# Optimization experiments

Hardware: AMD Instinct MI355X
Metric: run time of the kernel (lower is better)

## Reference

```python
import jax, jax.numpy as jnp
import numpy as np

B, IN_DIM, HID, OUT_DIM = 32768, 784, 256, 1000
L, CURV = 3, 1e-3
LOG2_H = 8  # log2(HID)
EPS_BN = 1e-5

def _layer_param_sizes():
    return [(HID // (2 * (1 << (l % LOG2_H)))) * 2 for l in range(L)]

def setup_inputs():
    key = jax.random.key(0)
    ks = jax.random.split(key, 4)
    total = sum(_layer_param_sizes())  # 448
    return {
        "x": jax.random.normal(ks[0], (B, IN_DIM), jnp.float32),
        "fc1_w": jax.random.normal(ks[1], (HID, IN_DIM), jnp.float32) / np.sqrt(IN_DIM).astype(np.float32),
        "fc1_b": jnp.zeros((HID,), jnp.float32),
        "bn1_gamma": jnp.ones((HID,), jnp.float32),
        "bn1_beta": jnp.zeros((HID,), jnp.float32),
        "bf_params": jax.random.normal(ks[2], (total,), jnp.float32) * 0.01,
        "bn2_gamma": jnp.ones((HID,), jnp.float32),
        "bn2_beta": jnp.zeros((HID,), jnp.float32),
        "fc2_w": jax.random.normal(ks[3], (OUT_DIM, HID), jnp.float32) / np.sqrt(HID).astype(np.float32),
        "fc2_b": jnp.zeros((OUT_DIM,), jnp.float32),
    }

def _batchnorm(h, gamma, beta):
    # training-mode BatchNorm1d: batch mean / biased variance
    mu = jnp.mean(h, axis=0)
    var = jnp.mean(jnp.square(h - mu), axis=0)
    return gamma * (h - mu) * jax.lax.rsqrt(var + EPS_BN) + beta

def _log_map0(x, c):
    # Poincare ball log map at origin: artanh(sqrt(c)|x|) * x / (sqrt(c)|x|)
    sn = jnp.sqrt(c) * jnp.linalg.norm(x, axis=-1, keepdims=True)
    sn = jnp.clip(sn, 1e-7, 1.0 - 1e-6)
    return (jnp.arctanh(sn) / sn) * x

def _exp_map0(u, c):
    sn = jnp.maximum(jnp.sqrt(c) * jnp.linalg.norm(u, axis=-1, keepdims=True), 1e-7)
    return (jnp.tanh(sn) / sn) * u

def _hyper_butterfly(h, params, c):
    u = _log_map0(h, c)
    off = 0
    for l in range(L):
        bs = 1 << (l % LOG2_H)      # half-block size at stage l
        nb = HID // (2 * bs)        # number of 2x2-rotation blocks
        p = params[off:off + 2 * nb]
        a = p[:nb][None, :, None]   # [1, nb, 1]
        b = p[nb:][None, :, None]
        v = u.reshape(-1, nb, 2, bs)
        x1, x2 = v[:, :, 0], v[:, :, 1]
        y1 = a * x1 + b * x2
        y2 = -b * x1 + a * x2
        u = jnp.stack([y1, y2], axis=2).reshape(-1, HID)
        off += 2 * nb
    return _exp_map0(u, c)

def reference(x, fc1_w, fc1_b, bn1_gamma, bn1_beta, bf_params, bn2_gamma, bn2_beta, fc2_w, fc2_b):
    h = x @ fc1_w.T + fc1_b
    h = jax.nn.relu(_batchnorm(h, bn1_gamma, bn1_beta))
    ht = _hyper_butterfly(h, bf_params, CURV)
    ht = jax.nn.relu(_batchnorm(ht, bn2_gamma, bn2_beta))
    return ht @ fc2_w.T + fc2_b
```

## Files before the change

kernel.cpp:

```cpp
#include <hip/hip_runtime.h>
#include <math.h>

#define NBATCH 32768
#define IND    784
#define KPAD1  800
#define HIDD   256
#define OUTD   1000
#define OUTDP  1024

typedef _Float16 half8  __attribute__((ext_vector_type(8)));
typedef _Float16 half4v __attribute__((ext_vector_type(4)));
typedef float    floatx4 __attribute__((ext_vector_type(4)));

#define GAS __attribute__((address_space(1)))
#define LAS __attribute__((address_space(3)))

#define WAITVM(N) asm volatile("s_waitcnt vmcnt(" #N ")" ::: "memory")
#define WAITVM_BAR(N)                                                      \
    asm volatile("s_waitcnt vmcnt(" #N ") lgkmcnt(0)" ::: "memory");       \
    __builtin_amdgcn_s_barrier();                                          \
    __builtin_amdgcn_sched_barrier(0)

__device__ __forceinline__ void gld16(const void* g, void* l) {
    __builtin_amdgcn_global_load_lds((const GAS void*)g, (LAS void*)l, 16, 0, 0);
}

__device__ __forceinline__ float wave_allreduce_sum(float v) {
    #pragma unroll
    for (int off = 32; off >= 1; off >>= 1) v += __shfl_xor(v, off);
    return v;
}

__global__ __launch_bounds__(256)
void prep_kernel(const float* __restrict__ w1, _Float16* __restrict__ w1h,
                 const float* __restrict__ w2, _Float16* __restrict__ w2h,
                 float* __restrict__ stat)
{
    const int tid = threadIdx.x;
    if (blockIdx.x == 0) {
        for (int j = tid; j < 1024 + 16; j += 256) stat[j] = 0.0f;
    }
    const int NW1 = HIDD * (KPAD1 / 8);
    const int NW2 = OUTDP * (HIDD / 8);
    for (int i = blockIdx.x * 256 + tid; i < NW1 + NW2; i += (int)gridDim.x * 256) {
        half8 o;
        if (i < NW1) {
            const int r = i / (KPAD1 / 8), c8 = (i % (KPAD1 / 8)) * 8;
            if (c8 + 8 <= IND) {
                const float* s = &w1[(size_t)r * IND + c8];
                float4 v0 = *(const float4*)s, v1 = *(const float4*)(s + 4);
                o[0]=(_Float16)v0.x; o[1]=(_Float16)v0.y; o[2]=(_Float16)v0.z; o[3]=(_Float16)v0.w;
                o[4]=(_Float16)v1.x; o[5]=(_Float16)v1.y; o[6]=(_Float16)v1.z; o[7]=(_Float16)v1.w;
            } else {
                #pragma unroll
                for (int j = 0; j < 8; ++j) o[j] = (_Float16)0.0f;
            }
            *(half8*)&w1h[(size_t)r * KPAD1 + c8] = o;
        } else {
            const int k = i - NW1;
            const int r = k >> 5, c8 = (k & 31) * 8;
            if (r < OUTD) {
                const float* s = &w2[(size_t)r * HIDD + c8];
                float4 v0 = *(const float4*)s, v1 = *(const float4*)(s + 4);
                o[0]=(_Float16)v0.x; o[1]=(_Float16)v0.y; o[2]=(_Float16)v0.z; o[3]=(_Float16)v0.w;
                o[4]=(_Float16)v1.x; o[5]=(_Float16)v1.y; o[6]=(_Float16)v1.z; o[7]=(_Float16)v1.w;
            } else {
                #pragma unroll
                for (int j = 0; j < 8; ++j) o[j] = (_Float16)0.0f;
            }
            *(half8*)&w2h[(size_t)r * HIDD + c8] = o;
        }
    }
}

__global__ __launch_bounds__(256, 3)
void gemm1_kernel(const float* __restrict__ x, const _Float16* __restrict__ w1h,
                  const float* __restrict__ b1, const float* __restrict__ zbuf,
                  _Float16* __restrict__ h16, float* __restrict__ sum1, float* __restrict__ ssq1)
{
    __shared__ __align__(16) _Float16 ldsA[2][4096];
    __shared__ __align__(16) _Float16 ldsB[3][4096];
    __shared__ float redS[2][128], redQ[2][128];

    const int tid  = threadIdx.x;
    const int bid0 = blockIdx.x;
    const int vbid = (bid0 & 7) * 64 + (bid0 >> 3);
    const int bm = vbid >> 1, bn = vbid & 1;
    const int m0 = bm * 128, n0 = bn * 128;
    const int lane = tid & 63, wv = tid >> 6;
    const int wr = wv >> 1, wc = wv & 1;
    const int l15 = lane & 15, lg = lane >> 4;
    const int e3 = l15 & 3;
    const int nt = KPAD1 / 32;

    const int r0g = tid >> 2;
    const int r1g = 64 + (tid >> 2);
    const int kq  = tid & 3;
    const int wpos0 = r0g * 32 + ((kq ^ (r0g & 3)) * 8);
    const int wpos1 = r1g * 32 + ((kq ^ (r1g & 3)) * 8);
    const float* Ab0 = x + (size_t)(m0 + r0g) * IND + kq * 8;
    const float* Ab1 = x + (size_t)(m0 + r1g) * IND + kq * 8;

    const int brow = lane >> 2, bgp = (lane & 3) ^ (brow & 3);
    const _Float16* Bb = w1h + (size_t)(n0 + brow) * KPAD1 + bgp * 8;

    floatx4 acc[4][4];
    #pragma unroll
    for (int i = 0; i < 4; ++i)
        #pragma unroll
        for (int j = 0; j < 4; ++j) acc[i][j] = (floatx4){0.f, 0.f, 0.f, 0.f};

    floatx4 rgaE[4], rgaO[4];

    auto A_ISSUE = [&](floatx4 (&rg)[4], int t) {
        const int t32 = t * 32;
        const bool v = (t32 + kq * 8) < IND;
        const float* p0 = v ? (Ab0 + t32) : zbuf;
        const float* p1 = v ? (Ab1 + t32) : zbuf;
        rg[0] = *(const floatx4*)p0;
        rg[1] = *(const floatx4*)(p0 + 4);
        rg[2] = *(const floatx4*)p1;
        rg[3] = *(const floatx4*)(p1 + 4);
    };
    auto A_WRITE = [&](floatx4 (&rg)[4], int wb) {
        half8 h0, h1;
        #pragma unroll
        for (int j = 0; j < 4; ++j) {
            h0[j] = (_Float16)rg[0][j]; h0[4 + j] = (_Float16)rg[1][j];
            h1[j] = (_Float16)rg[2][j]; h1[4 + j] = (_Float16)rg[3][j];
        }
        *(half8*)&ldsA[wb][wpos0] = h0;
        *(half8*)&ldsA[wb][wpos1] = h1;
    };
    auto B_ISSUE = [&](int bb, int t) {
        const int t32 = t * 32;
        const bool tok = t < nt;
        #pragma unroll
        for (int c = 0; c < 2; ++c) {
            const int ch = wv + c * 4;
            const void* s = tok ? (const void*)(Bb + (size_t)ch * 16 * KPAD1 + t32)
                                : (const void*)zbuf;
            gld16(s, &ldsB[bb][ch * 512]);
        }
    };

    auto COMPUTE = [&](int abuf, int brd) {
        half8 af[4], bfr[4];
        #pragma unroll
        for (int i = 0; i < 4; ++i)
            af[i] = *(const half8*)&ldsA[abuf][(wr * 64 + i * 16 + l15) * 32 + ((lg ^ e3) * 8)];
        #pragma unroll
        for (int j = 0; j < 4; ++j)
            bfr[j] = *(const half8*)&ldsB[brd][(wc * 4 + j) * 512 + l15 * 32 + ((lg ^ e3) * 8)];
        #pragma unroll
        for (int i = 0; i < 4; ++i)
            #pragma unroll
            for (int j = 0; j < 4; ++j)
                acc[i][j] = __builtin_amdgcn_mfma_f32_16x16x32_f16(bfr[j], af[i], acc[i][j], 0, 0, 0);
    };

    A_ISSUE(rgaE, 0); B_ISSUE(0, 0);
    WAITVM(2);
    A_WRITE(rgaE, 0);
    A_ISSUE(rgaO, 1); B_ISSUE(1, 1);
    WAITVM_BAR(6);

    int b0 = 0;
    for (int p = 0; p < 12; ++p) {
        const int t  = p * 2;
        const int b1v = b0 + 1 == 3 ? 0 : b0 + 1;
        const int b2v = b1v + 1 == 3 ? 0 : b1v + 1;
        A_ISSUE(rgaE, t + 2);
        B_ISSUE(b2v, t + 2);
        COMPUTE(0, b0);
        __builtin_amdgcn_sched_barrier(0);
        WAITVM(6);
        A_WRITE(rgaO, 1);
        WAITVM_BAR(6);
        A_ISSUE(rgaO, t + 3);
        B_ISSUE(b0, t + 3);
        COMPUTE(1, b1v);
        __builtin_amdgcn_sched_barrier(0);
        WAITVM(6);
        A_WRITE(rgaE, 0);
        WAITVM_BAR(6);
        b0 = b2v;
    }
    COMPUTE(0, b0);
    WAITVM(0);

    float sJ[4][4], qJ[4][4];
    #pragma unroll
    for (int j = 0; j < 4; ++j)
        #pragma unroll
        for (int r = 0; r < 4; ++r) { sJ[j][r] = 0.f; qJ[j][r] = 0.f; }
    #pragma unroll
    for (int i = 0; i < 4; ++i) {
        const int m = m0 + wr * 64 + i * 16 + l15;
        #pragma unroll
        for (int j = 0; j < 4; ++j) {
            const int nb = n0 + wc * 64 + j * 16 + lg * 4;
            float4 bt = *reinterpret_cast<const float4*>(&b1[nb]);
            float v[4] = {acc[i][j][0] + bt.x, acc[i][j][1] + bt.y,
                          acc[i][j][2] + bt.z, acc[i][j][3] + bt.w};
            half4v hv;
            hv[0] = (_Float16)v[0]; hv[1] = (_Float16)v[1];
            hv[2] = (_Float16)v[2]; hv[3] = (_Float16)v[3];
            *reinterpret_cast<half4v*>(&h16[(size_t)m * HIDD + nb]) = hv;
            #pragma unroll
            for (int r = 0; r < 4; ++r) { sJ[j][r] += v[r]; qJ[j][r] += v[r] * v[r]; }
        }
    }
    #pragma unroll
    for (int j = 0; j < 4; ++j)
        #pragma unroll
        for (int r = 0; r < 4; ++r) {
            float s = sJ[j][r], q = qJ[j][r];
            s += __shfl_xor(s, 1); s += __shfl_xor(s, 2);
            s += __shfl_xor(s, 4); s += __shfl_xor(s, 8);
            q += __shfl_xor(q, 1); q += __shfl_xor(q, 2);
            q += __shfl_xor(q, 4); q += __shfl_xor(q, 8);
            if (l15 == 0) {
                redS[wr][wc * 64 + j * 16 + lg * 4 + r] = s;
                redQ[wr][wc * 64 + j * 16 + lg * 4 + r] = q;
            }
        }
    __syncthreads();
    if (tid < 128) {
        atomicAdd(&sum1[n0 + tid], redS[0][tid] + redS[1][tid]);
        atomicAdd(&ssq1[n0 + tid], redQ[0][tid] + redQ[1][tid]);
    }
}

__global__ __launch_bounds__(256)
void mid_kernel(const _Float16* __restrict__ h16, const float* __restrict__ bfp,
                const float* __restrict__ sum1, const float* __restrict__ ssq1,
                const float* __restrict__ g1, const float* __restrict__ be1,
                _Float16* __restrict__ ht16, float* __restrict__ sum2, float* __restrict__ ssq2)
{
    __shared__ float s1sh[256], t1sh[256];
    __shared__ float bsum[4][256], bssq[4][256];
    const int tid  = threadIdx.x;
    {
        const float inv = 1.0f / (float)NBATCH;
        const float mu  = sum1[tid] * inv;
        const float var = fmaxf(ssq1[tid] * inv - mu * mu, 0.0f);
        const float rs  = 1.0f / sqrtf(var + 1e-5f);
        const float sj  = g1[tid] * rs;
        s1sh[tid] = sj;
        t1sh[tid] = fmaf(-mu, sj, be1[tid]);
    }
    __syncthreads();

    const int w    = tid >> 6;
    const int lane = tid & 63;
    const int row0 = blockIdx.x * 64 + w * 16;
    const int c0   = lane * 4;

    const float4 s1v = *reinterpret_cast<const float4*>(&s1sh[c0]);
    const float4 t1v = *reinterpret_cast<const float4*>(&t1sh[c0]);
    const float a0 = bfp[2 * lane],       a1 = bfp[2 * lane + 1];
    const float b0 = bfp[128 + 2 * lane], b1 = bfp[128 + 2 * lane + 1];
    const float a2 = bfp[256 + lane],     b2 = bfp[320 + lane];
    const float a3 = bfp[384 + (lane >> 1)], b3 = bfp[416 + (lane >> 1)];
    const float sgn = (lane & 1) ? -1.0f : 1.0f;
    const float sc  = sqrtf(1e-3f);

    float ps0 = 0, ps1 = 0, ps2 = 0, ps3 = 0;
    float q0 = 0, q1 = 0, q2 = 0, q3 = 0;

    for (int r = 0; r < 16; ++r) {
        const int row = row0 + r;
        half4v hv4 = *reinterpret_cast<const half4v*>(&h16[(size_t)row * HIDD + c0]);
        float x0 = fmaxf(fmaf((float)hv4[0], s1v.x, t1v.x), 0.0f);
        float x1 = fmaxf(fmaf((float)hv4[1], s1v.y, t1v.y), 0.0f);
        float x2 = fmaxf(fmaf((float)hv4[2], s1v.z, t1v.z), 0.0f);
        float x3 = fmaxf(fmaf((float)hv4[3], s1v.w, t1v.w), 0.0f);
        float n2 = x0 * x0 + x1 * x1 + x2 * x2 + x3 * x3;
        n2 = wave_allreduce_sum(n2);
        float sn = sc * sqrtf(n2);
        sn = fminf(fmaxf(sn, 1e-7f), 1.0f - 1e-6f);
        const float ls = atanhf(sn) / sn;
        x0 *= ls; x1 *= ls; x2 *= ls; x3 *= ls;
        const float y0 = fmaf(a0, x0,  b0 * x1);
        const float y1 = fmaf(a0, x1, -b0 * x0);
        const float y2 = fmaf(a1, x2,  b1 * x3);
        const float y3 = fmaf(a1, x3, -b1 * x2);
        const float z0 = fmaf(a2, y0,  b2 * y2);
        const float z1 = fmaf(a2, y1,  b2 * y3);
        const float z2 = fmaf(a2, y2, -b2 * y0);
        const float z3 = fmaf(a2, y3, -b2 * y1);
        const float p0 = __shfl_xor(z0, 1);
        const float p1 = __shfl_xor(z1, 1);
        const float p2 = __shfl_xor(z2, 1);
        const float p3 = __shfl_xor(z3, 1);
        const float w0 = fmaf(a3, z0, sgn * (b3 * p0));
        const float w1 = fmaf(a3, z1, sgn * (b3 * p1));
        const float w2 = fmaf(a3, z2, sgn * (b3 * p2));
        const float w3 = fmaf(a3, z3, sgn * (b3 * p3));
        float m2 = w0 * w0 + w1 * w1 + w2 * w2 + w3 * w3;
        m2 = wave_allreduce_sum(m2);
        const float sn2 = fmaxf(sc * sqrtf(m2), 1e-7f);
        const float es = tanhf(sn2) / sn2;
        const float o0 = es * w0, o1 = es * w1, o2 = es * w2, o3 = es * w3;
        half4v hv;
        hv[0] = (_Float16)(o0 * 65536.0f); hv[1] = (_Float16)(o1 * 65536.0f);
        hv[2] = (_Float16)(o2 * 65536.0f); hv[3] = (_Float16)(o3 * 65536.0f);
        *reinterpret_cast<half4v*>(&ht16[(size_t)row * HIDD + c0]) = hv;
        ps0 += o0; ps1 += o1; ps2 += o2; ps3 += o3;
        q0 += o0 * o0; q1 += o1 * o1; q2 += o2 * o2; q3 += o3 * o3;
    }

    bsum[w][c0 + 0] = ps0; bsum[w][c0 + 1] = ps1; bsum[w][c0 + 2] = ps2; bsum[w][c0 + 3] = ps3;
    bssq[w][c0 + 0] = q0;  bssq[w][c0 + 1] = q1;  bssq[w][c0 + 2] = q2;  bssq[w][c0 + 3] = q3;
    __syncthreads();
    if (tid < 256) {
        const float s = bsum[0][tid] + bsum[1][tid] + bsum[2][tid] + bsum[3][tid];
        const float q = bssq[0][tid] + bssq[1][tid] + bssq[2][tid] + bssq[3][tid];
        atomicAdd(&sum2[tid], s);
        atomicAdd(&ssq2[tid], q);
    }
}

__global__ __launch_bounds__(256, 3)
void gemm2_kernel(const _Float16* __restrict__ ht16, const _Float16* __restrict__ w2h,
                  const float* __restrict__ b2,
                  const float* __restrict__ sum2, const float* __restrict__ ssq2,
                  const float* __restrict__ g2, const float* __restrict__ be2,
                  const float* __restrict__ zbuf, float* __restrict__ out)
{
    __shared__ __align__(16) _Float16 ldsA[3][4096];
    __shared__ __align__(16) _Float16 ldsB[3][4096];
    __shared__ float sf[256], tf[256];

    const int tid = threadIdx.x;
    {
        const float inv = 1.0f / (float)NBATCH;
        const float mu  = sum2[tid] * inv;
        const float var = fmaxf(ssq2[tid] * inv - mu * mu, 0.0f);
        const float rs  = 1.0f / sqrtf(var + 1e-5f);
        const float sj  = g2[tid] * rs;
        sf[tid] = sj * (1024.0f / 65536.0f);
        tf[tid] = fmaf(-mu, sj, be2[tid]) * 1024.0f;
    }

    const int bid0 = blockIdx.x;
    const int vbid = (bid0 & 7) * 256 + (bid0 >> 3);
    const int bm = vbid >> 3, bn = vbid & 7;
    const int m0 = bm * 128, n0 = bn * 128;
    const int lane = tid & 63, wv = tid >> 6;
    const int wr = wv >> 1, wc = wv & 1;
    const int l15 = lane & 15, lg = lane >> 4;
    const int e3 = l15 & 3;
    const int nt = HIDD / 32;

    const int srow = lane >> 2, sgp = (lane & 3) ^ (srow & 3);
    const _Float16* Ab = ht16 + (size_t)(m0 + srow) * HIDD + sgp * 8;
    const _Float16* Bb = w2h  + (size_t)(n0 + srow) * HIDD + sgp * 8;

    floatx4 acc[4][4];
    #pragma unroll
    for (int i = 0; i < 4; ++i)
        #pragma unroll
        for (int j = 0; j < 4; ++j) acc[i][j] = (floatx4){0.f, 0.f, 0.f, 0.f};

    auto STAGE = [&](int buf, int t) {
        const int t32 = t * 32;
        const bool tok = t < nt;
        #pragma unroll
        for (int c = 0; c < 2; ++c) {
            const int ch = wv + c * 4;
            const void* sa = tok ? (const void*)(Ab + (size_t)ch * 16 * HIDD + t32)
                                 : (const void*)zbuf;
            const void* sb = tok ? (const void*)(Bb + (size_t)ch * 16 * HIDD + t32)
                                 : (const void*)zbuf;
            gld16(sa, &ldsA[buf][ch * 512]);
            gld16(sb, &ldsB[buf][ch * 512]);
        }
    };

    STAGE(0, 0);
    STAGE(1, 1);
    WAITVM_BAR(4);

    int buf = 0;
    for (int t = 0; t < nt; ++t) {
        int nbuf = buf + 2; if (nbuf >= 3) nbuf -= 3;
        STAGE(nbuf, t + 2);
        const int kb = t * 32 + lg * 8;
        float4 s0 = *(const float4*)&sf[kb], s1 = *(const float4*)&sf[kb + 4];
        float4 t0 = *(const float4*)&tf[kb], t1 = *(const float4*)&tf[kb + 4];
        half8 af[4], bfr[4];
        #pragma unroll
        for (int i = 0; i < 4; ++i) {
            half8 v = *(const half8*)&ldsA[buf][(wr * 4 + i) * 512 + l15 * 32 + ((lg ^ e3) * 8)];
            half8 hv;
            hv[0] = (_Float16)fmaxf(fmaf((float)v[0], s0.x, t0.x), 0.0f);
            hv[1] = (_Float16)fmaxf(fmaf((float)v[1], s0.y, t0.y), 0.0f);
            hv[2] = (_Float16)fmaxf(fmaf((float)v[2], s0.z, t0.z), 0.0f);
            hv[3] = (_Float16)fmaxf(fmaf((float)v[3], s0.w, t0.w), 0.0f);
            hv[4] = (_Float16)fmaxf(fmaf((float)v[4], s1.x, t1.x), 0.0f);
            hv[5] = (_Float16)fmaxf(fmaf((float)v[5], s1.y, t1.y), 0.0f);
            hv[6] = (_Float16)fmaxf(fmaf((float)v[6], s1.z, t1.z), 0.0f);
            hv[7] = (_Float16)fmaxf(fmaf((float)v[7], s1.w, t1.w), 0.0f);
            af[i] = hv;
        }
        #pragma unroll
        for (int j = 0; j < 4; ++j)
            bfr[j] = *(const half8*)&ldsB[buf][(wc * 4 + j) * 512 + l15 * 32 + ((lg ^ e3) * 8)];
        #pragma unroll
        for (int i = 0; i < 4; ++i)
            #pragma unroll
            for (int j = 0; j < 4; ++j)
                acc[i][j] = __builtin_amdgcn_mfma_f32_16x16x32_f16(bfr[j], af[i], acc[i][j], 0, 0, 0);
        WAITVM_BAR(4);
        buf = (buf + 1 == 3) ? 0 : buf + 1;
    }
    WAITVM(0);

    const float invScale = 1.0f / 1024.0f;
    #pragma unroll
    for (int i = 0; i < 4; ++i) {
        const int m = m0 + wr * 64 + i * 16 + l15;
        #pragma unroll
        for (int j = 0; j < 4; ++j) {
            const int nb = n0 + wc * 64 + j * 16 + lg * 4;
            float bj[4];
            if (nb + 4 <= OUTD) {
                float4 bt = *reinterpret_cast<const float4*>(&b2[nb]);
                bj[0] = bt.x; bj[1] = bt.y; bj[2] = bt.z; bj[3] = bt.w;
            } else {
                #pragma unroll
                for (int r = 0; r < 4; ++r) bj[r] = (nb + r < OUTD) ? b2[nb + r] : 0.0f;
            }
            float v[4];
            #pragma unroll
            for (int r = 0; r < 4; ++r) v[r] = fmaf(acc[i][j][r], invScale, bj[r]);
            if (nb + 4 <= OUTD) {
                *reinterpret_cast<float4*>(&out[(size_t)m * OUTD + nb]) =
                    make_float4(v[0], v[1], v[2], v[3]);
            } else {
                #pragma unroll
                for (int r = 0; r < 4; ++r)
                    if (nb + r < OUTD) out[(size_t)m * OUTD + nb + r] = v[r];
            }
        }
    }
}

extern "C" void kernel_launch(void* const* d_in, const int* in_sizes, int n_in,
                              void* d_out, int out_size, void* d_ws, size_t ws_size,
                              hipStream_t stream)
{
    const float* x   = (const float*)d_in[0];
    const float* w1  = (const float*)d_in[1];
    const float* b1  = (const float*)d_in[2];
    const float* g1  = (const float*)d_in[3];
    const float* be1 = (const float*)d_in[4];
    const float* bfp = (const float*)d_in[5];
    const float* g2  = (const float*)d_in[6];
    const float* be2 = (const float*)d_in[7];
    const float* w2  = (const float*)d_in[8];
    const float* b2  = (const float*)d_in[9];

    float* out = (float*)d_out;
    char*  wsb = (char*)d_ws;

    _Float16* ht16 = (_Float16*)(wsb);
    _Float16* w1h  = (_Float16*)(wsb + 16777216);
    _Float16* w2h  = (_Float16*)(wsb + 17186816);
    float*    stat = (float*)  (wsb + 17711104);
    float* sum1 = stat;
    float* ssq1 = stat + 256;
    float* sum2 = stat + 512;
    float* ssq2 = stat + 768;
    float* zbuf = stat + 1024;

    _Float16* h16 = (_Float16*)out;

    prep_kernel<<<232, 256, 0, stream>>>(w1, w1h, w2, w2h, stat);
    gemm1_kernel<<<512, 256, 0, stream>>>(x, w1h, b1, zbuf, h16, sum1, ssq1);
    mid_kernel<<<512, 256, 0, stream>>>(h16, bfp, sum1, ssq1, g1, be1, ht16, sum2, ssq2);
    gemm2_kernel<<<2048, 256, 0, stream>>>(ht16, w2h, b2, sum2, ssq2, g2, be2, zbuf, out);
}
```

Baseline: 127.2 us.

## Double K-tile depth in gemm1 and switch B to double buffering

The fc1 GEMM now processes 64-wide K tiles (two 32-wide MFMA sub-steps) per pipeline stage instead of 32. This halves the number of barrier and wait synchronisations per block. K padding rises to 832, and B moves from a triple-buffered ring to a fixed double buffer with a reordered issue schedule. The larger LDS footprint and extra staging registers drop the occupancy target from 3 to 2 blocks per CU, which may reduce latency hiding. The zero-padded tail tile also adds some wasted work.

```diff
diff --git a/kernel.cpp b/kernel.cpp
--- a/kernel.cpp
+++ b/kernel.cpp
@@ -3,7 +3,7 @@
 
 #define NBATCH 32768
 #define IND    784
-#define KPAD1  800
+#define KPAD1  832
 #define HIDD   256
 #define OUTD   1000
 #define OUTDP  1024
@@ -73,13 +73,13 @@
     }
 }
 
-__global__ __launch_bounds__(256, 3)
+__global__ __launch_bounds__(256, 2)
 void gemm1_kernel(const float* __restrict__ x, const _Float16* __restrict__ w1h,
                   const float* __restrict__ b1, const float* __restrict__ zbuf,
                   _Float16* __restrict__ h16, float* __restrict__ sum1, float* __restrict__ ssq1)
 {
-    __shared__ __align__(16) _Float16 ldsA[2][4096];
-    __shared__ __align__(16) _Float16 ldsB[3][4096];
+    __shared__ __align__(16) _Float16 ldsA[2][8192];
+    __shared__ __align__(16) _Float16 ldsB[2][8192];
     __shared__ float redS[2][128], redQ[2][128];
 
     const int tid  = threadIdx.x;
@@ -91,11 +91,9 @@
     const int wr = wv >> 1, wc = wv & 1;
     const int l15 = lane & 15, lg = lane >> 4;
     const int e3 = l15 & 3;
-    const int nt = KPAD1 / 32;
-
-    const int r0g = tid >> 2;
-    const int r1g = 64 + (tid >> 2);
-    const int kq  = tid & 3;
+    const int nt = KPAD1 / 64;
+
+    const int r0g = tid >> 2, r1g = 64 + (tid >> 2), kq = tid & 3;
     const int wpos0 = r0g * 32 + ((kq ^ (r0g & 3)) * 8);
     const int wpos1 = r1g * 32 + ((kq ^ (r1g & 3)) * 8);
     const float* Ab0 = x + (size_t)(m0 + r0g) * IND + kq * 8;
@@ -110,83 +108,89 @@
         #pragma unroll
         for (int j = 0; j < 4; ++j) acc[i][j] = (floatx4){0.f, 0.f, 0.f, 0.f};
 
-    floatx4 rgaE[4], rgaO[4];
-
-    auto A_ISSUE = [&](floatx4 (&rg)[4], int t) {
-        const int t32 = t * 32;
-        const bool v = (t32 + kq * 8) < IND;
-        const float* p0 = v ? (Ab0 + t32) : zbuf;
-        const float* p1 = v ? (Ab1 + t32) : zbuf;
-        rg[0] = *(const floatx4*)p0;
-        rg[1] = *(const floatx4*)(p0 + 4);
-        rg[2] = *(const floatx4*)p1;
-        rg[3] = *(const floatx4*)(p1 + 4);
+    floatx4 rgaE[8], rgaO[8];
+
+    auto A_ISSUE = [&](floatx4 (&rg)[8], int t) {
+        #pragma unroll
+        for (int ks = 0; ks < 2; ++ks) {
+            const int off = t * 64 + ks * 32;
+            const bool v = (off + kq * 8) < IND;
+            const float* p0 = v ? (Ab0 + off) : zbuf;
+            const float* p1 = v ? (Ab1 + off) : zbuf;
+            rg[ks*4+0] = *(const floatx4*)p0;
+            rg[ks*4+1] = *(const floatx4*)(p0 + 4);
+            rg[ks*4+2] = *(const floatx4*)p1;
+            rg[ks*4+3] = *(const floatx4*)(p1 + 4);
+        }
     };
-    auto A_WRITE = [&](floatx4 (&rg)[4], int wb) {
-        half8 h0, h1;
-        #pragma unroll
-        for (int j = 0; j < 4; ++j) {
-            h0[j] = (_Float16)rg[0][j]; h0[4 + j] = (_Float16)rg[1][j];
-            h1[j] = (_Float16)rg[2][j]; h1[4 + j] = (_Float16)rg[3][j];
-        }
-        *(half8*)&ldsA[wb][wpos0] = h0;
-        *(half8*)&ldsA[wb][wpos1] = h1;
+    auto A_WRITE = [&](floatx4 (&rg)[8], int wb) {
+        #pragma unroll
+        for (int ks = 0; ks < 2; ++ks) {
+            half8 h0, h1;
+            #pragma unroll
+            for (int j = 0; j < 4; ++j) {
+                h0[j] = (_Float16)rg[ks*4+0][j]; h0[4+j] = (_Float16)rg[ks*4+1][j];
+                h1[j] = (_Float16)rg[ks*4+2][j]; h1[4+j] = (_Float16)rg[ks*4+3][j];
+            }
+            *(half8*)&ldsA[wb][ks * 4096 + wpos0] = h0;
+            *(half8*)&ldsA[wb][ks * 4096 + wpos1] = h1;
+        }
     };
     auto B_ISSUE = [&](int bb, int t) {
-        const int t32 = t * 32;
         const bool tok = t < nt;
         #pragma unroll
-        for (int c = 0; c < 2; ++c) {
-            const int ch = wv + c * 4;
-            const void* s = tok ? (const void*)(Bb + (size_t)ch * 16 * KPAD1 + t32)
-                                : (const void*)zbuf;
-            gld16(s, &ldsB[bb][ch * 512]);
-        }
+        for (int ks = 0; ks < 2; ++ks)
+            #pragma unroll
+            for (int c = 0; c < 2; ++c) {
+                const int ch = wv + c * 4;
+                const void* s = tok ? (const void*)(Bb + (size_t)ch * 16 * KPAD1 + t * 64 + ks * 32)
+                                    : (const void*)zbuf;
+                gld16(s, &ldsB[bb][ks * 4096 + ch * 512]);
+            }
     };
-
     auto COMPUTE = [&](int abuf, int brd) {
-        half8 af[4], bfr[4];
-        #pragma unroll
-        for (int i = 0; i < 4; ++i)
-            af[i] = *(const half8*)&ldsA[abuf][(wr * 64 + i * 16 + l15) * 32 + ((lg ^ e3) * 8)];
-        #pragma unroll
-        for (int j = 0; j < 4; ++j)
-            bfr[j] = *(const half8*)&ldsB[brd][(wc * 4 + j) * 512 + l15 * 32 + ((lg ^ e3) * 8)];
-        #pragma unroll
-        for (int i = 0; i < 4; ++i)
+        #pragma unroll
+        for (int ks = 0; ks < 2; ++ks) {
+            half8 af[4], bfr[4];
+            #pragma unroll
+            for (int i = 0; i < 4; ++i)
+                af[i] = *(const half8*)&ldsA[abuf][ks*4096 + (wr*64 + i*16 + l15)*32 + ((lg ^ e3)*8)];
             #pragma unroll
             for (int j = 0; j < 4; ++j)
-                acc[i][j] = __builtin_amdgcn_mfma_f32_16x16x32_f16(bfr[j], af[i], acc[i][j], 0, 0, 0);
+                bfr[j] = *(const half8*)&ldsB[brd][ks*4096 + (wc*4 + j)*512 + l15*32 + ((lg ^ e3)*8)];
+            #pragma unroll
+            for (int i = 0; i < 4; ++i)
+                #pragma unroll
+                for (int j = 0; j < 4; ++j)
+                    acc[i][j] = __builtin_amdgcn_mfma_f32_16x16x32_f16(bfr[j], af[i], acc[i][j], 0, 0, 0);
+        }
     };
 
-    A_ISSUE(rgaE, 0); B_ISSUE(0, 0);
-    WAITVM(2);
+    A_ISSUE(rgaE, 0);
+    B_ISSUE(0, 0);
+    WAITVM(4);
     A_WRITE(rgaE, 0);
-    A_ISSUE(rgaO, 1); B_ISSUE(1, 1);
-    WAITVM_BAR(6);
-
-    int b0 = 0;
-    for (int p = 0; p < 12; ++p) {
-        const int t  = p * 2;
-        const int b1v = b0 + 1 == 3 ? 0 : b0 + 1;
-        const int b2v = b1v + 1 == 3 ? 0 : b1v + 1;
+    A_ISSUE(rgaO, 1);
+    WAITVM_BAR(8);
+
+    for (int p = 0; p < 6; ++p) {
+        const int t = p * 2;
+        B_ISSUE(1, t + 1);
         A_ISSUE(rgaE, t + 2);
-        B_ISSUE(b2v, t + 2);
-        COMPUTE(0, b0);
+        COMPUTE(0, 0);
         __builtin_amdgcn_sched_barrier(0);
-        WAITVM(6);
+        WAITVM(8);
         A_WRITE(rgaO, 1);
-        WAITVM_BAR(6);
+        WAITVM_BAR(8);
+        B_ISSUE(0, t + 2);
         A_ISSUE(rgaO, t + 3);
-        B_ISSUE(b0, t + 3);
-        COMPUTE(1, b1v);
+        COMPUTE(1, 1);
         __builtin_amdgcn_sched_barrier(0);
-        WAITVM(6);
+        WAITVM(8);
         A_WRITE(rgaE, 0);
-        WAITVM_BAR(6);
-        b0 = b2v;
-    }
-    COMPUTE(0, b0);
+        WAITVM_BAR(8);
+    }
+    COMPUTE(0, 0);
     WAITVM(0);
 
     float sJ[4][4], qJ[4][4];
@@ -468,8 +472,8 @@
 
     _Float16* ht16 = (_Float16*)(wsb);
     _Float16* w1h  = (_Float16*)(wsb + 16777216);
-    _Float16* w2h  = (_Float16*)(wsb + 17186816);
-    float*    stat = (float*)  (wsb + 17711104);
+    _Float16* w2h  = (_Float16*)(wsb + 17203200);
+    float*    stat = (float*)  (wsb + 17727488);
     float* sum1 = stat;
     float* ssq1 = stat + 256;
     float* sum2 = stat + 512;
```

Result: no change. 126.9 us (-0.2%).
